# Optimization experiments

Hardware: AMD Instinct MI355X
Metric: run time of the kernel (lower is better)

## Reference

```python
import jax, jax.numpy as jnp
import numpy as np
import math

N_HEAD = 16
N_EMBD = 1024
N_LATENTS = 64
HEAD_DIM = N_EMBD // N_HEAD  # 64
ROPE_THETA = 10000.0


def setup_inputs() -> dict:
    key = jax.random.key(0)
    ks = jax.random.split(key, 6)
    B, T = 4, 4096
    x = jax.random.normal(ks[0], (B, T, N_EMBD), dtype=jnp.float32)
    # torch Linear weights applied as x @ W with W: [in, out] (equivalent up to init)
    s = 1.0 / math.sqrt(N_EMBD)
    Wk = jax.random.normal(ks[1], (N_EMBD, N_EMBD), dtype=jnp.float32) * s
    Wv = jax.random.normal(ks[2], (N_EMBD, N_EMBD), dtype=jnp.float32) * s
    Wg = jax.random.normal(ks[3], (N_EMBD, N_HEAD * N_LATENTS), dtype=jnp.float32) * s
    Wp = jax.random.normal(ks[4], (N_EMBD, N_EMBD), dtype=jnp.float32) * s
    latent_q = jax.random.normal(ks[5], (1, N_LATENTS, N_HEAD, HEAD_DIM), dtype=jnp.float32)
    return {"x": x, "latent_q": latent_q, "Wk": Wk, "Wv": Wv, "Wg": Wg, "Wp": Wp}


def _rope_interleaved(k, theta):
    # k: [B, T, H, D]; interleaved pairs rotated by position-dependent angles
    B, T, H, D = k.shape
    inv_freq = 1.0 / (theta ** (jnp.arange(0, D, 2, dtype=jnp.float32) / D))  # [D/2]
    ang = jnp.arange(T, dtype=jnp.float32)[:, None] * inv_freq[None, :]       # [T, D/2]
    cos = jnp.cos(ang)[None, :, None, :]
    sin = jnp.sin(ang)[None, :, None, :]
    k2 = k.reshape(B, T, H, D // 2, 2)
    kr = jnp.stack([k2[..., 0] * cos - k2[..., 1] * sin,
                    k2[..., 0] * sin + k2[..., 1] * cos], axis=-1)
    return kr.reshape(B, T, H, D).astype(k.dtype)


def reference(x, latent_q, Wk, Wv, Wg, Wp):
    B, T, C = x.shape
    H, D, L = N_HEAD, HEAD_DIM, N_LATENTS
    k = (x @ Wk).reshape(B, T, H, D)
    v = (x @ Wv).reshape(B, T, H, D)
    gates = jax.nn.softmax((x @ Wg).reshape(B, T, H, L), axis=-1)  # [B,T,H,L]
    k = _rope_interleaved(k, ROPE_THETA)
    q = jnp.broadcast_to(latent_q, (B, L, H, D)).transpose(0, 2, 1, 3)  # [B,H,L,D]
    kt = k.transpose(0, 2, 1, 3)  # [B,H,T,D]
    vt = v.transpose(0, 2, 1, 3)  # [B,H,T,D]
    scale = 1.0 / jnp.sqrt(jnp.asarray(D, dtype=x.dtype))
    scores = jnp.einsum('bhld,bhtd->bhlt', q, kt) * scale  # [B,H,L,T]
    # PyTorch SDPA is_causal with L_q != L_kv: top-left aligned tril(ones(L, T))
    causal = jnp.arange(T)[None, :] <= jnp.arange(L)[:, None]  # [L,T]
    scores = jnp.where(causal[None, None], scores, -jnp.inf)
    attn = jax.nn.softmax(scores, axis=-1)
    attn_out = jnp.einsum('bhlt,bhtd->bhld', attn, vt)  # [B,H,L,D]
    gates_t = gates.transpose(0, 2, 1, 3)  # [B,H,T,L]
    weighted = jnp.einsum('bhld,bhtl->bhtd', attn_out, gates_t)  # [B,H,T,D]
    out = weighted.transpose(0, 2, 1, 3).reshape(B, T, C)
    return out @ Wp
```

## Files before the change

### kernel.cpp

```cpp
#include <hip/hip_runtime.h>
#include <hip/hip_bf16.h>


typedef __attribute__((ext_vector_type(8))) short bf16x8;
typedef __attribute__((ext_vector_type(4))) float f32x4;
typedef __attribute__((ext_vector_type(4))) unsigned short us4;
typedef __attribute__((ext_vector_type(8))) unsigned short us8;

__device__ __forceinline__ void gll16(const void* g, void* l) {
  __builtin_amdgcn_global_load_lds((const __attribute__((address_space(1))) void*)g,
                                   (__attribute__((address_space(3))) void*)l, 16, 0, 0);
}

__global__ __launch_bounds__(256)
void prep_kernel(const float* __restrict__ x, __hip_bfloat16* __restrict__ xb,
                 const float* __restrict__ Wg, const float* __restrict__ Wk,
                 const float* __restrict__ Wv, const float* __restrict__ Wp,
                 __hip_bfloat16* __restrict__ WgT, __hip_bfloat16* __restrict__ WkT,
                 __hip_bfloat16* __restrict__ WvT, __hip_bfloat16* __restrict__ WpT) {
  const int bid = blockIdx.x, tid = threadIdx.x;
  if (bid < 2048) {
    const int stride = 2048 * 256;
    for (int i = bid * 256 + tid; i < 4194304; i += stride) {
      float4 f = reinterpret_cast<const float4*>(x)[i];
      union { __hip_bfloat16 h[4]; us4 v; } u;
      u.h[0] = __float2bfloat16(f.x);
      u.h[1] = __float2bfloat16(f.y);
      u.h[2] = __float2bfloat16(f.z);
      u.h[3] = __float2bfloat16(f.w);
      reinterpret_cast<us4*>(xb)[i] = u.v;
    }
  } else {
    const int t = bid - 2048;
    const int z = t >> 10, rem = t & 1023;
    const float* W = (z == 0) ? Wg : ((z == 1) ? Wk : ((z == 2) ? Wv : Wp));
    __hip_bfloat16* Wt = (z == 0) ? WgT : ((z == 1) ? WkT : ((z == 2) ? WvT : WpT));
    __shared__ float tile[32][33];
    const int bx = (rem & 31) * 32, by = (rem >> 5) * 32;
    const int tx = tid & 31, ty = tid >> 5;
    #pragma unroll
    for (int j = 0; j < 32; j += 8)
      tile[ty + j][tx] = W[(size_t)(by + ty + j) * 1024 + bx + tx];
    __syncthreads();
    #pragma unroll
    for (int j = 0; j < 32; j += 8)
      Wt[(size_t)(bx + ty + j) * 1024 + by + tx] = __float2bfloat16(tile[tx][ty + j]);
  }
}

template <int EPI>
__global__ __launch_bounds__(512, 2)
void gemm256(const __hip_bfloat16* __restrict__ A, const __hip_bfloat16* __restrict__ Bt,
             void* __restrict__ Cv, int K, int ldc,
             long long astride, long long bstride, long long cstride) {
  __shared__ __align__(16) unsigned short SA[2][256 * 64];
  __shared__ __align__(16) unsigned short SB[2][256 * 64];
  const int tid = threadIdx.x;
  const int lane = tid & 63;
  const int w = tid >> 6;
  const int wm = w >> 2, wn = w & 3;
  const int lr = lane & 15, lk = lane >> 4;
  const int m0 = blockIdx.x * 256, n0 = blockIdx.y * 256;
  const long long b = blockIdx.z;
  const __hip_bfloat16* Ab = A + b * astride;
  const __hip_bfloat16* Bb = Bt + b * bstride;

  f32x4 acc[8][4] = {};

  const int NT = K >> 6;
  int buf = 0;

  auto STAGE = [&](int bsel, int kt) {
    #pragma unroll
    for (int r = 0; r < 4; ++r) {
      int c = r * 512 + tid;
      int row = c >> 3, slot = c & 7;
      int gch = slot ^ (row & 7);
      gll16(Ab + (size_t)(m0 + row) * K + kt + gch * 8, (char*)&SA[bsel][0] + c * 16);
      gll16(Bb + (size_t)(n0 + row) * K + kt + gch * 8, (char*)&SB[bsel][0] + c * 16);
    }
  };

  STAGE(0, 0);
  __syncthreads();

  for (int t = 0; t < NT; ++t) {
    if (t + 1 < NT) STAGE(buf ^ 1, (t + 1) << 6);

    bf16x8 bfr[2][4];
    #pragma unroll
    for (int kk = 0; kk < 2; ++kk)
      #pragma unroll
      for (int ni = 0; ni < 4; ++ni) {
        int row = wn * 64 + ni * 16 + lr;
        int ch = (kk * 4 + lk) ^ (row & 7);
        bfr[kk][ni] = *(const bf16x8*)&SB[buf][row * 64 + ch * 8];
      }
    #pragma unroll
    for (int mi = 0; mi < 8; ++mi) {
      int row = wm * 128 + mi * 16 + lr;
      int ch0 = lk ^ (row & 7);
      int ch1 = (4 + lk) ^ (row & 7);
      bf16x8 a0 = *(const bf16x8*)&SA[buf][row * 64 + ch0 * 8];
      bf16x8 a1 = *(const bf16x8*)&SA[buf][row * 64 + ch1 * 8];
      #pragma unroll
      for (int ni = 0; ni < 4; ++ni)
        acc[mi][ni] = __builtin_amdgcn_mfma_f32_16x16x32_bf16(a0, bfr[0][ni], acc[mi][ni], 0, 0, 0);
      #pragma unroll
      for (int ni = 0; ni < 4; ++ni)
        acc[mi][ni] = __builtin_amdgcn_mfma_f32_16x16x32_bf16(a1, bfr[1][ni], acc[mi][ni], 0, 0, 0);
    }
    __syncthreads();
    buf ^= 1;
  }

  if (EPI == 0) {
    float* C = (float*)Cv + b * cstride;
    #pragma unroll
    for (int mi = 0; mi < 8; ++mi) {
      int r = m0 + wm * 128 + mi * 16 + lk * 4;
      #pragma unroll
      for (int ni = 0; ni < 4; ++ni) {
        int c = n0 + wn * 64 + ni * 16 + lr;
        #pragma unroll
        for (int jj = 0; jj < 4; ++jj)
          C[(size_t)(r + jj) * ldc + c] = acc[mi][ni][jj];
      }
    }
  } else {
    __hip_bfloat16* C = (__hip_bfloat16*)Cv + b * cstride;
    #pragma unroll
    for (int mi = 0; mi < 8; ++mi) {
      #pragma unroll
      for (int jj = 0; jj < 4; ++jj) {
        float mx = -3.0e38f;
        #pragma unroll
        for (int ni = 0; ni < 4; ++ni) mx = fmaxf(mx, acc[mi][ni][jj]);
        mx = fmaxf(mx, __shfl_xor(mx, 1));
        mx = fmaxf(mx, __shfl_xor(mx, 2));
        mx = fmaxf(mx, __shfl_xor(mx, 4));
        mx = fmaxf(mx, __shfl_xor(mx, 8));
        float e[4];
        float s = 0.f;
        #pragma unroll
        for (int ni = 0; ni < 4; ++ni) { e[ni] = __expf(acc[mi][ni][jj] - mx); s += e[ni]; }
        s += __shfl_xor(s, 1);
        s += __shfl_xor(s, 2);
        s += __shfl_xor(s, 4);
        s += __shfl_xor(s, 8);
        float inv = 1.0f / s;
        int r = m0 + wm * 128 + mi * 16 + lk * 4 + jj;
        #pragma unroll
        for (int ni = 0; ni < 4; ++ni)
          C[(size_t)r * ldc + n0 + wn * 64 + ni * 16 + lr] = __float2bfloat16(e[ni] * inv);
      }
    }
  }
}

__global__ __launch_bounds__(256)
void gemm_kv(const __hip_bfloat16* __restrict__ A, const __hip_bfloat16* __restrict__ Bt,
             float* __restrict__ kvp) {
  __shared__ __align__(16) unsigned short As[128 * 32];
  __shared__ __align__(16) unsigned short Bs[128 * 32];
  const int tid = threadIdx.x;
  const int lane = tid & 63;
  const int w = tid >> 6;
  const int wm = w >> 1, wn = w & 1;
  const int lr = lane & 15, lk = lane >> 4;
  const int m0 = blockIdx.x * 128, n0 = blockIdx.y * 128;
  const int ks = blockIdx.z;
  const int K = 1024;

  f32x4 acc[4][4] = {};
  const int r0 = tid >> 2;
  const int c8 = (tid & 3) * 8;

  auto xrow = [&](int rg) { return (size_t)(rg >> 6) * 4096 + (rg & 63); };

  for (int ki = 0; ki < 4; ++ki) {
    int kt = ks * 128 + ki * 32;
    __syncthreads();
    gll16(A + xrow(m0 + r0) * K + kt + c8,      (char*)As + (w * 64) * 16);
    gll16(Bt + (size_t)(n0 + r0) * K + kt + c8, (char*)Bs + (w * 64) * 16);
    gll16(A + xrow(m0 + 64 + r0) * K + kt + c8,      (char*)As + (256 + w * 64) * 16);
    gll16(Bt + (size_t)(n0 + 64 + r0) * K + kt + c8, (char*)Bs + (256 + w * 64) * 16);
    __syncthreads();

    bf16x8 af[4], bf[4];
    #pragma unroll
    for (int mi = 0; mi < 4; ++mi)
      af[mi] = *(const bf16x8*)&As[(wm * 64 + mi * 16 + lr) * 32 + lk * 8];
    #pragma unroll
    for (int ni = 0; ni < 4; ++ni)
      bf[ni] = *(const bf16x8*)&Bs[(wn * 64 + ni * 16 + lr) * 32 + lk * 8];
    #pragma unroll
    for (int mi = 0; mi < 4; ++mi)
      #pragma unroll
      for (int ni = 0; ni < 4; ++ni)
        acc[mi][ni] = __builtin_amdgcn_mfma_f32_16x16x32_bf16(af[mi], bf[ni], acc[mi][ni], 0, 0, 0);
  }

  float* C = kvp + (size_t)ks * 256 * 2048;
  #pragma unroll
  for (int mi = 0; mi < 4; ++mi) {
    int r = m0 + wm * 64 + mi * 16 + lk * 4;
    #pragma unroll
    for (int ni = 0; ni < 4; ++ni) {
      int c = n0 + wn * 64 + ni * 16 + lr;
      #pragma unroll
      for (int jj = 0; jj < 4; ++jj)
        C[(size_t)(r + jj) * 2048 + c] = acc[mi][ni][jj];
    }
  }
}

__global__ __launch_bounds__(256)
void attn_kernel(const float* __restrict__ kvp, const float* __restrict__ lq,
                 __hip_bfloat16* __restrict__ aoB) {
  const int h = blockIdx.x, b = blockIdx.y;
  __shared__ float Ks[64][64];
  __shared__ float Vs[64][64];
  __shared__ float S[64][65];
  __shared__ float Pt[64][65];
  const int tid = threadIdx.x;

  {
    int r = tid >> 4;
    int c4 = (tid & 15) * 4;
    int i0 = c4 >> 1;
    float inv0 = exp2f(-13.287712379549449f * ((float)i0 * (1.0f / 32.0f)));
    float inv1 = exp2f(-13.287712379549449f * ((float)(i0 + 1) * (1.0f / 32.0f)));
    #pragma unroll
    for (int j = 0; j < 4; ++j) {
      int row = j * 16 + r;
      float4 kf = make_float4(0.f, 0.f, 0.f, 0.f);
      float4 vf = make_float4(0.f, 0.f, 0.f, 0.f);
      #pragma unroll
      for (int ks = 0; ks < 8; ++ks) {
        const float* base = kvp + ((size_t)ks * 256 + b * 64 + row) * 2048 + h * 64;
        float4 kp = *(const float4*)(base + c4);
        float4 vp = *(const float4*)(base + 1024 + c4);
        kf.x += kp.x; kf.y += kp.y; kf.z += kp.z; kf.w += kp.w;
        vf.x += vp.x; vf.y += vp.y; vf.z += vp.z; vf.w += vp.w;
      }
      float a0 = (float)row * inv0, a1 = (float)row * inv1;
      float s0 = sinf(a0), c0 = cosf(a0), s1 = sinf(a1), c1 = cosf(a1);
      *(float4*)&Ks[row][c4] = make_float4(kf.x * c0 - kf.y * s0, kf.x * s0 + kf.y * c0,
                                           kf.z * c1 - kf.w * s1, kf.z * s1 + kf.w * c1);
      *(float4*)&Vs[row][c4] = vf;
    }
  }
  __syncthreads();

  {
    const int w = tid >> 6, l = tid & 63;
    float q[64];
    const float4* lq4 = (const float4*)(lq + ((size_t)l * 16 + h) * 64);
    #pragma unroll
    for (int i = 0; i < 16; ++i) {
      float4 f = lq4[i];
      q[4 * i] = f.x; q[4 * i + 1] = f.y; q[4 * i + 2] = f.z; q[4 * i + 3] = f.w;
    }
    #pragma unroll
    for (int tl = 0; tl < 16; ++tl) {
      int t = w * 16 + tl;
      float a = 0.f;
      #pragma unroll
      for (int d4 = 0; d4 < 16; ++d4) {
        float4 kf = *(const float4*)&Ks[t][d4 * 4];
        a += q[4 * d4] * kf.x + q[4 * d4 + 1] * kf.y + q[4 * d4 + 2] * kf.z + q[4 * d4 + 3] * kf.w;
      }
      S[l][t] = a * 0.125f;
    }
  }
  __syncthreads();

  {
    const int l = tid >> 2, c = tid & 3;
    float sv[16];
    float mx = -3.0e38f;
    #pragma unroll
    for (int i = 0; i < 16; ++i) {
      int t = c * 16 + i;
      sv[i] = S[l][t];
      if (t <= l) mx = fmaxf(mx, sv[i]);
    }
    mx = fmaxf(mx, __shfl_xor(mx, 1));
    mx = fmaxf(mx, __shfl_xor(mx, 2));
    float sum = 0.f;
    float e[16];
    #pragma unroll
    for (int i = 0; i < 16; ++i) {
      int t = c * 16 + i;
      e[i] = (t <= l) ? __expf(sv[i] - mx) : 0.f;
      sum += e[i];
    }
    sum += __shfl_xor(sum, 1);
    sum += __shfl_xor(sum, 2);
    float inv = 1.0f / sum;
    #pragma unroll
    for (int i = 0; i < 16; ++i) Pt[c * 16 + i][l] = e[i] * inv;
  }
  __syncthreads();

  {
    const int w = tid >> 6, l = tid & 63;
    float o[16];
    #pragma unroll
    for (int i = 0; i < 16; ++i) o[i] = 0.f;
    for (int t = 0; t < 64; ++t) {
      float p = Pt[t][l];
      #pragma unroll
      for (int d4 = 0; d4 < 4; ++d4) {
        float4 vf = *(const float4*)&Vs[t][w * 16 + d4 * 4];
        o[4 * d4]     += p * vf.x;
        o[4 * d4 + 1] += p * vf.y;
        o[4 * d4 + 2] += p * vf.z;
        o[4 * d4 + 3] += p * vf.w;
      }
    }
    union { __hip_bfloat16 h[16]; us8 v[2]; } u;
    #pragma unroll
    for (int i = 0; i < 16; ++i) u.h[i] = __float2bfloat16(o[i]);
    us8* dst = (us8*)(aoB + (((size_t)b * 16 + h) * 64 + l) * 64 + w * 16);
    dst[0] = u.v[0];
    dst[1] = u.v[1];
  }
}

__global__ __launch_bounds__(256)
void build_mt_mfma(const __hip_bfloat16* __restrict__ aoB, const __hip_bfloat16* __restrict__ WpT,
                   __hip_bfloat16* __restrict__ Mt) {
  __shared__ __align__(16) unsigned short SW[256 * 64];
  __shared__ __align__(16) unsigned short SAo[64 * 64];
  const int ct = blockIdx.x, h = blockIdx.y, b = blockIdx.z;
  const int tid = threadIdx.x;
  const int lane = tid & 63;
  const int w = tid >> 6;
  const int lr = lane & 15, lk = lane >> 4;

  #pragma unroll
  for (int j = 0; j < 8; ++j) {
    int c2 = j * 256 + tid;
    int row = c2 >> 3, slot = c2 & 7;
    int gch = slot ^ (row & 7);
    gll16(WpT + (size_t)(ct * 256 + row) * 1024 + h * 64 + gch * 8, (char*)SW + c2 * 16);
  }
  const __hip_bfloat16* aob = aoB + (((size_t)b * 16 + h) * 64) * 64;
  #pragma unroll
  for (int j = 0; j < 2; ++j) {
    int c2 = j * 256 + tid;
    int row = c2 >> 3, slot = c2 & 7;
    int gch = slot ^ (row & 7);
    gll16(aob + (size_t)row * 64 + gch * 8, (char*)SAo + c2 * 16);
  }
  __syncthreads();

  f32x4 acc[4][4] = {};
  bf16x8 bfr[2][4];
  #pragma unroll
  for (int kk = 0; kk < 2; ++kk)
    #pragma unroll
    for (int ni = 0; ni < 4; ++ni) {
      int row = ni * 16 + lr;
      int ch = (kk * 4 + lk) ^ (row & 7);
      bfr[kk][ni] = *(const bf16x8*)&SAo[row * 64 + ch * 8];
    }
  #pragma unroll
  for (int mi = 0; mi < 4; ++mi) {
    int row = w * 64 + mi * 16 + lr;
    int ch0 = lk ^ (row & 7);
    int ch1 = (4 + lk) ^ (row & 7);
    bf16x8 a0 = *(const bf16x8*)&SW[row * 64 + ch0 * 8];
    bf16x8 a1 = *(const bf16x8*)&SW[row * 64 + ch1 * 8];
    #pragma unroll
    for (int ni = 0; ni < 4; ++ni)
      acc[mi][ni] = __builtin_amdgcn_mfma_f32_16x16x32_bf16(a0, bfr[0][ni], acc[mi][ni], 0, 0, 0);
    #pragma unroll
    for (int ni = 0; ni < 4; ++ni)
      acc[mi][ni] = __builtin_amdgcn_mfma_f32_16x16x32_bf16(a1, bfr[1][ni], acc[mi][ni], 0, 0, 0);
  }

  #pragma unroll
  for (int mi = 0; mi < 4; ++mi) {
    int c = ct * 256 + w * 64 + mi * 16 + lk * 4;
    #pragma unroll
    for (int ni = 0; ni < 4; ++ni) {
      int l = ni * 16 + lr;
      #pragma unroll
      for (int jj = 0; jj < 4; ++jj)
        Mt[((size_t)b * 1024 + c + jj) * 1024 + h * 64 + l] = __float2bfloat16(acc[mi][ni][jj]);
    }
  }
}

extern "C" void kernel_launch(void* const* d_in, const int* in_sizes, int n_in,
                              void* d_out, int out_size, void* d_ws, size_t ws_size,
                              hipStream_t stream) {
  const float* x  = (const float*)d_in[0];
  const float* lq = (const float*)d_in[1];
  const float* Wk = (const float*)d_in[2];
  const float* Wv = (const float*)d_in[3];
  const float* Wg = (const float*)d_in[4];
  const float* Wp = (const float*)d_in[5];
  float* out = (float*)d_out;

  char* w = (char*)d_ws;
  __hip_bfloat16* xb   = (__hip_bfloat16*)(w);
  __hip_bfloat16* G    = (__hip_bfloat16*)(w + 33554432);
  __hip_bfloat16* WgT  = (__hip_bfloat16*)(w + 67108864);
  __hip_bfloat16* WkvT = (__hip_bfloat16*)(w + 69206016);
  __hip_bfloat16* WpT  = (__hip_bfloat16*)(w + 73400320);
  __hip_bfloat16* Mt   = (__hip_bfloat16*)(w + 75497472);
  __hip_bfloat16* aoB  = (__hip_bfloat16*)(w + 83886080);
  float* kvp = out;

  prep_kernel<<<6144, 256, 0, stream>>>(x, xb, Wg, Wk, Wv, Wp,
                                        WgT, WkvT, WkvT + 1024 * 1024, WpT);

  gemm256<1><<<dim3(64, 4, 1), 512, 0, stream>>>(xb, WgT, G, 1024, 1024, 0LL, 0LL, 0LL);

  gemm_kv<<<dim3(2, 16, 8), 256, 0, stream>>>(xb, WkvT, kvp);

  attn_kernel<<<dim3(16, 4), 256, 0, stream>>>(kvp, lq, aoB);

  build_mt_mfma<<<dim3(4, 16, 4), 256, 0, stream>>>(aoB, WpT, Mt);

  gemm256<0><<<dim3(16, 4, 4), 512, 0, stream>>>(G, Mt, out, 1024, 1024,
                                                 4096LL * 1024, 1024LL * 1024, 4096LL * 1024);
}
```

Measured before the change: 132.3 us.

## Fuse fp32-to-bf16 conversion of x into gates and KV GEMM loaders

Removes the separate pass that converted x to a bf16 workspace copy. The gates GEMM now stages fp32 x tiles into LDS via direct global-to-LDS loads and converts them to bf16 in shared memory inside a double-buffered pipeline. The KV GEMM loads fp32 x into registers and converts before writing LDS. This drops the 32MB bf16 write and reread of x, but doubles the bytes each GEMM reads for A, adds LDS usage, and the gates kernel loses its 2-blocks occupancy hint and uses a smaller K tile.

```diff
diff --git a/kernel.cpp b/kernel.cpp
--- a/kernel.cpp
+++ b/kernel.cpp
@@ -13,46 +13,150 @@
 }
 
 __global__ __launch_bounds__(256)
-void prep_kernel(const float* __restrict__ x, __hip_bfloat16* __restrict__ xb,
-                 const float* __restrict__ Wg, const float* __restrict__ Wk,
-                 const float* __restrict__ Wv, const float* __restrict__ Wp,
-                 __hip_bfloat16* __restrict__ WgT, __hip_bfloat16* __restrict__ WkT,
-                 __hip_bfloat16* __restrict__ WvT, __hip_bfloat16* __restrict__ WpT) {
+void prep4(const float* __restrict__ Wg, const float* __restrict__ Wk,
+           const float* __restrict__ Wv, const float* __restrict__ Wp,
+           __hip_bfloat16* __restrict__ WgT, __hip_bfloat16* __restrict__ WkT,
+           __hip_bfloat16* __restrict__ WvT, __hip_bfloat16* __restrict__ WpT) {
   const int bid = blockIdx.x, tid = threadIdx.x;
-  if (bid < 2048) {
-    const int stride = 2048 * 256;
-    for (int i = bid * 256 + tid; i < 4194304; i += stride) {
-      float4 f = reinterpret_cast<const float4*>(x)[i];
-      union { __hip_bfloat16 h[4]; us4 v; } u;
-      u.h[0] = __float2bfloat16(f.x);
-      u.h[1] = __float2bfloat16(f.y);
-      u.h[2] = __float2bfloat16(f.z);
-      u.h[3] = __float2bfloat16(f.w);
-      reinterpret_cast<us4*>(xb)[i] = u.v;
-    }
-  } else {
-    const int t = bid - 2048;
-    const int z = t >> 10, rem = t & 1023;
-    const float* W = (z == 0) ? Wg : ((z == 1) ? Wk : ((z == 2) ? Wv : Wp));
-    __hip_bfloat16* Wt = (z == 0) ? WgT : ((z == 1) ? WkT : ((z == 2) ? WvT : WpT));
-    __shared__ float tile[32][33];
-    const int bx = (rem & 31) * 32, by = (rem >> 5) * 32;
-    const int tx = tid & 31, ty = tid >> 5;
-    #pragma unroll
-    for (int j = 0; j < 32; j += 8)
-      tile[ty + j][tx] = W[(size_t)(by + ty + j) * 1024 + bx + tx];
+  const int z = bid >> 10, rem = bid & 1023;
+  const float* W = (z == 0) ? Wg : ((z == 1) ? Wk : ((z == 2) ? Wv : Wp));
+  __hip_bfloat16* Wt = (z == 0) ? WgT : ((z == 1) ? WkT : ((z == 2) ? WvT : WpT));
+  __shared__ float tile[32][33];
+  const int bx = (rem & 31) * 32, by = (rem >> 5) * 32;
+  const int tx = tid & 31, ty = tid >> 5;
+  #pragma unroll
+  for (int j = 0; j < 32; j += 8)
+    tile[ty + j][tx] = W[(size_t)(by + ty + j) * 1024 + bx + tx];
+  __syncthreads();
+  #pragma unroll
+  for (int j = 0; j < 32; j += 8)
+    Wt[(size_t)(bx + ty + j) * 1024 + by + tx] = __float2bfloat16(tile[tx][ty + j]);
+}
+
+__global__ __launch_bounds__(512)
+void gemm_gates_f32(const float* __restrict__ X, const __hip_bfloat16* __restrict__ Bt,
+                    __hip_bfloat16* __restrict__ G) {
+  __shared__ __align__(16) float SF[2][256 * 32];
+  __shared__ __align__(16) unsigned short SA16[2][256 * 32];
+  __shared__ __align__(16) unsigned short SB[2][256 * 32];
+  const int tid = threadIdx.x;
+  const int lane = tid & 63;
+  const int w = tid >> 6;
+  const int wm = w >> 2, wn = w & 3;
+  const int lr = lane & 15, lk = lane >> 4;
+  const int m0 = blockIdx.x * 256, n0 = blockIdx.y * 256;
+  const int K = 1024;
+
+  f32x4 acc[8][4] = {};
+
+  auto stageF = [&](int bsel, int kt) {
+    #pragma unroll
+    for (int r = 0; r < 4; ++r) {
+      int c = r * 512 + tid;
+      int row = c >> 3, p = c & 7;
+      int gs = p ^ (row & 7);
+      gll16(X + (size_t)(m0 + row) * K + kt + gs * 4, (char*)&SF[bsel][0] + c * 16);
+    }
+  };
+  auto stageB = [&](int bsel, int kt) {
+    #pragma unroll
+    for (int r = 0; r < 2; ++r) {
+      int c = r * 512 + tid;
+      int row2 = c >> 3, p = c & 7;
+      int l = p ^ (row2 & 7);
+      int row = row2 * 2 + (l >> 2);
+      int s4 = l & 3;
+      gll16(Bt + (size_t)(n0 + row) * K + kt + s4 * 8, (char*)&SB[bsel][0] + c * 16);
+    }
+  };
+  auto convert = [&](int bsel) {
+    #pragma unroll
+    for (int r = 0; r < 2; ++r) {
+      int c = r * 512 + tid;
+      int row2 = c >> 3, p = c & 7;
+      int l = p ^ (row2 & 7);
+      int row = row2 * 2 + (l >> 2);
+      int s4 = l & 3;
+      int f0 = (2 * s4) ^ (row & 7);
+      int f1 = (2 * s4 + 1) ^ (row & 7);
+      float4 a  = *(const float4*)&SF[bsel][row * 32 + f0 * 4];
+      float4 b2 = *(const float4*)&SF[bsel][row * 32 + f1 * 4];
+      union { __hip_bfloat16 h[8]; bf16x8 v; } pk;
+      pk.h[0] = __float2bfloat16(a.x);  pk.h[1] = __float2bfloat16(a.y);
+      pk.h[2] = __float2bfloat16(a.z);  pk.h[3] = __float2bfloat16(a.w);
+      pk.h[4] = __float2bfloat16(b2.x); pk.h[5] = __float2bfloat16(b2.y);
+      pk.h[6] = __float2bfloat16(b2.z); pk.h[7] = __float2bfloat16(b2.w);
+      *(bf16x8*)&SA16[bsel][c * 8] = pk.v;
+    }
+  };
+
+  stageF(0, 0);
+  stageB(0, 0);
+  __syncthreads();
+  convert(0);
+  stageF(1, 32);
+  __syncthreads();
+
+  const int NT = 32;
+  for (int t = 0; t < NT; ++t) {
+    if (t + 2 < NT) stageF(t & 1, (t + 2) * 32);
+    if (t + 1 < NT) {
+      stageB((t + 1) & 1, (t + 1) * 32);
+      convert((t + 1) & 1);
+    }
+
+    const int buf = t & 1;
+    bf16x8 bfr[4];
+    #pragma unroll
+    for (int ni = 0; ni < 4; ++ni) {
+      int row = wn * 64 + ni * 16 + lr;
+      int ch = ((row >> 1) * 8) + ((((row & 1) << 2) | lk) ^ ((row >> 1) & 7));
+      bfr[ni] = *(const bf16x8*)&SB[buf][ch * 8];
+    }
+    #pragma unroll
+    for (int mi = 0; mi < 8; ++mi) {
+      int row = wm * 128 + mi * 16 + lr;
+      int ch = ((row >> 1) * 8) + ((((row & 1) << 2) | lk) ^ ((row >> 1) & 7));
+      bf16x8 a = *(const bf16x8*)&SA16[buf][ch * 8];
+      #pragma unroll
+      for (int ni = 0; ni < 4; ++ni)
+        acc[mi][ni] = __builtin_amdgcn_mfma_f32_16x16x32_bf16(a, bfr[ni], acc[mi][ni], 0, 0, 0);
+    }
     __syncthreads();
-    #pragma unroll
-    for (int j = 0; j < 32; j += 8)
-      Wt[(size_t)(bx + ty + j) * 1024 + by + tx] = __float2bfloat16(tile[tx][ty + j]);
-  }
-}
-
-template <int EPI>
+  }
+
+  #pragma unroll
+  for (int mi = 0; mi < 8; ++mi) {
+    #pragma unroll
+    for (int jj = 0; jj < 4; ++jj) {
+      float mx = -3.0e38f;
+      #pragma unroll
+      for (int ni = 0; ni < 4; ++ni) mx = fmaxf(mx, acc[mi][ni][jj]);
+      mx = fmaxf(mx, __shfl_xor(mx, 1));
+      mx = fmaxf(mx, __shfl_xor(mx, 2));
+      mx = fmaxf(mx, __shfl_xor(mx, 4));
+      mx = fmaxf(mx, __shfl_xor(mx, 8));
+      float e[4];
+      float s = 0.f;
+      #pragma unroll
+      for (int ni = 0; ni < 4; ++ni) { e[ni] = __expf(acc[mi][ni][jj] - mx); s += e[ni]; }
+      s += __shfl_xor(s, 1);
+      s += __shfl_xor(s, 2);
+      s += __shfl_xor(s, 4);
+      s += __shfl_xor(s, 8);
+      float inv = 1.0f / s;
+      int r = m0 + wm * 128 + mi * 16 + lk * 4 + jj;
+      #pragma unroll
+      for (int ni = 0; ni < 4; ++ni)
+        G[(size_t)r * 1024 + n0 + wn * 64 + ni * 16 + lr] = __float2bfloat16(e[ni] * inv);
+    }
+  }
+}
+
 __global__ __launch_bounds__(512, 2)
-void gemm256(const __hip_bfloat16* __restrict__ A, const __hip_bfloat16* __restrict__ Bt,
-             void* __restrict__ Cv, int K, int ldc,
-             long long astride, long long bstride, long long cstride) {
+void gemm256o(const __hip_bfloat16* __restrict__ A, const __hip_bfloat16* __restrict__ Bt,
+              float* __restrict__ Cv, int K, int ldc,
+              long long astride, long long bstride, long long cstride) {
   __shared__ __align__(16) unsigned short SA[2][256 * 64];
   __shared__ __align__(16) unsigned short SB[2][256 * 64];
   const int tid = threadIdx.x;
@@ -114,52 +218,22 @@
     buf ^= 1;
   }
 
-  if (EPI == 0) {
-    float* C = (float*)Cv + b * cstride;
-    #pragma unroll
-    for (int mi = 0; mi < 8; ++mi) {
-      int r = m0 + wm * 128 + mi * 16 + lk * 4;
-      #pragma unroll
-      for (int ni = 0; ni < 4; ++ni) {
-        int c = n0 + wn * 64 + ni * 16 + lr;
-        #pragma unroll
-        for (int jj = 0; jj < 4; ++jj)
-          C[(size_t)(r + jj) * ldc + c] = acc[mi][ni][jj];
-      }
-    }
-  } else {
-    __hip_bfloat16* C = (__hip_bfloat16*)Cv + b * cstride;
-    #pragma unroll
-    for (int mi = 0; mi < 8; ++mi) {
-      #pragma unroll
-      for (int jj = 0; jj < 4; ++jj) {
-        float mx = -3.0e38f;
-        #pragma unroll
-        for (int ni = 0; ni < 4; ++ni) mx = fmaxf(mx, acc[mi][ni][jj]);
-        mx = fmaxf(mx, __shfl_xor(mx, 1));
-        mx = fmaxf(mx, __shfl_xor(mx, 2));
-        mx = fmaxf(mx, __shfl_xor(mx, 4));
-        mx = fmaxf(mx, __shfl_xor(mx, 8));
-        float e[4];
-        float s = 0.f;
-        #pragma unroll
-        for (int ni = 0; ni < 4; ++ni) { e[ni] = __expf(acc[mi][ni][jj] - mx); s += e[ni]; }
-        s += __shfl_xor(s, 1);
-        s += __shfl_xor(s, 2);
-        s += __shfl_xor(s, 4);
-        s += __shfl_xor(s, 8);
-        float inv = 1.0f / s;
-        int r = m0 + wm * 128 + mi * 16 + lk * 4 + jj;
-        #pragma unroll
-        for (int ni = 0; ni < 4; ++ni)
-          C[(size_t)r * ldc + n0 + wn * 64 + ni * 16 + lr] = __float2bfloat16(e[ni] * inv);
-      }
+  float* C = Cv + b * cstride;
+  #pragma unroll
+  for (int mi = 0; mi < 8; ++mi) {
+    int r = m0 + wm * 128 + mi * 16 + lk * 4;
+    #pragma unroll
+    for (int ni = 0; ni < 4; ++ni) {
+      int c = n0 + wn * 64 + ni * 16 + lr;
+      #pragma unroll
+      for (int jj = 0; jj < 4; ++jj)
+        C[(size_t)(r + jj) * ldc + c] = acc[mi][ni][jj];
     }
   }
 }
 
 __global__ __launch_bounds__(256)
-void gemm_kv(const __hip_bfloat16* __restrict__ A, const __hip_bfloat16* __restrict__ Bt,
+void gemm_kv(const float* __restrict__ X, const __hip_bfloat16* __restrict__ Bt,
              float* __restrict__ kvp) {
   __shared__ __align__(16) unsigned short As[128 * 32];
   __shared__ __align__(16) unsigned short Bs[128 * 32];
@@ -173,18 +247,36 @@
   const int K = 1024;
 
   f32x4 acc[4][4] = {};
-  const int r0 = tid >> 2;
-  const int c8 = (tid & 3) * 8;
 
   auto xrow = [&](int rg) { return (size_t)(rg >> 6) * 4096 + (rg & 63); };
 
   for (int ki = 0; ki < 4; ++ki) {
     int kt = ks * 128 + ki * 32;
     __syncthreads();
-    gll16(A + xrow(m0 + r0) * K + kt + c8,      (char*)As + (w * 64) * 16);
-    gll16(Bt + (size_t)(n0 + r0) * K + kt + c8, (char*)Bs + (w * 64) * 16);
-    gll16(A + xrow(m0 + 64 + r0) * K + kt + c8,      (char*)As + (256 + w * 64) * 16);
-    gll16(Bt + (size_t)(n0 + 64 + r0) * K + kt + c8, (char*)Bs + (256 + w * 64) * 16);
+    float4 av[4];
+    #pragma unroll
+    for (int r = 0; r < 2; ++r) {
+      int c = r * 256 + tid;
+      int row = c >> 2, s = c & 3;
+      const float* src = X + xrow(m0 + row) * K + kt + s * 8;
+      av[2 * r]     = *(const float4*)src;
+      av[2 * r + 1] = *(const float4*)(src + 4);
+    }
+    #pragma unroll
+    for (int r = 0; r < 2; ++r) {
+      int c = r * 256 + tid;
+      int row = c >> 2, s = c & 3;
+      gll16(Bt + (size_t)(n0 + row) * K + kt + s * 8, (char*)Bs + c * 16);
+    }
+    #pragma unroll
+    for (int r = 0; r < 2; ++r) {
+      int c = r * 256 + tid;
+      union { __hip_bfloat16 h[8]; bf16x8 v; } p;
+      const float* f = (const float*)&av[2 * r];
+      #pragma unroll
+      for (int e = 0; e < 8; ++e) p.h[e] = __float2bfloat16(f[e]);
+      *(bf16x8*)((char*)As + c * 16) = p.v;
+    }
     __syncthreads();
 
     bf16x8 af[4], bf[4];
@@ -407,26 +499,24 @@
   float* out = (float*)d_out;
 
   char* w = (char*)d_ws;
-  __hip_bfloat16* xb   = (__hip_bfloat16*)(w);
-  __hip_bfloat16* G    = (__hip_bfloat16*)(w + 33554432);
-  __hip_bfloat16* WgT  = (__hip_bfloat16*)(w + 67108864);
-  __hip_bfloat16* WkvT = (__hip_bfloat16*)(w + 69206016);
-  __hip_bfloat16* WpT  = (__hip_bfloat16*)(w + 73400320);
-  __hip_bfloat16* Mt   = (__hip_bfloat16*)(w + 75497472);
-  __hip_bfloat16* aoB  = (__hip_bfloat16*)(w + 83886080);
+  __hip_bfloat16* G    = (__hip_bfloat16*)(w);
+  __hip_bfloat16* WgT  = (__hip_bfloat16*)(w + 33554432);
+  __hip_bfloat16* WkvT = (__hip_bfloat16*)(w + 35651584);
+  __hip_bfloat16* WpT  = (__hip_bfloat16*)(w + 39845888);
+  __hip_bfloat16* Mt   = (__hip_bfloat16*)(w + 41943040);
+  __hip_bfloat16* aoB  = (__hip_bfloat16*)(w + 50331648);
   float* kvp = out;
 
-  prep_kernel<<<6144, 256, 0, stream>>>(x, xb, Wg, Wk, Wv, Wp,
-                                        WgT, WkvT, WkvT + 1024 * 1024, WpT);
-
-  gemm256<1><<<dim3(64, 4, 1), 512, 0, stream>>>(xb, WgT, G, 1024, 1024, 0LL, 0LL, 0LL);
-
-  gemm_kv<<<dim3(2, 16, 8), 256, 0, stream>>>(xb, WkvT, kvp);
+  prep4<<<4096, 256, 0, stream>>>(Wg, Wk, Wv, Wp, WgT, WkvT, WkvT + 1024 * 1024, WpT);
+
+  gemm_gates_f32<<<dim3(64, 4), 512, 0, stream>>>(x, WgT, G);
+
+  gemm_kv<<<dim3(2, 16, 8), 256, 0, stream>>>(x, WkvT, kvp);
 
   attn_kernel<<<dim3(16, 4), 256, 0, stream>>>(kvp, lq, aoB);
 
   build_mt_mfma<<<dim3(4, 16, 4), 256, 0, stream>>>(aoB, WpT, Mt);
 
-  gemm256<0><<<dim3(16, 4, 4), 512, 0, stream>>>(G, Mt, out, 1024, 1024,
-                                                 4096LL * 1024, 1024LL * 1024, 4096LL * 1024);
-}
+  gemm256o<<<dim3(16, 4, 4), 512, 0, stream>>>(G, Mt, out, 1024, 1024,
+                                               4096LL * 1024, 1024LL * 1024, 4096LL * 1024);
+}
```

Measured after the change: 137.1 us. +3.6%, slower.

## Fuse attention into Mt construction and swizzle GEMM block order

Applied to the files above, without the earlier changes.

Merges the attention kernel with the build-Mt kernel, so each block recomputes attention output for its (b,h) and writes it into shared memory instead of a global bf16 buffer. This removes one launch and the global round trip of the attention output. The attention work is now done redundantly four times, once per column tile. Separately, the two gemm256 launches switch to a 1D grid with an XCD-aware block swizzle (bid&7)*32+(bid>>3), aimed at better L2 locality across chiplets.

```diff
diff --git a/kernel.cpp b/kernel.cpp
--- a/kernel.cpp
+++ b/kernel.cpp
@@ -5,7 +5,6 @@
 typedef __attribute__((ext_vector_type(8))) short bf16x8;
 typedef __attribute__((ext_vector_type(4))) float f32x4;
 typedef __attribute__((ext_vector_type(4))) unsigned short us4;
-typedef __attribute__((ext_vector_type(8))) unsigned short us8;
 
 __device__ __forceinline__ void gll16(const void* g, void* l) {
   __builtin_amdgcn_global_load_lds((const __attribute__((address_space(1))) void*)g,
@@ -52,7 +51,8 @@
 __global__ __launch_bounds__(512, 2)
 void gemm256(const __hip_bfloat16* __restrict__ A, const __hip_bfloat16* __restrict__ Bt,
              void* __restrict__ Cv, int K, int ldc,
-             long long astride, long long bstride, long long cstride) {
+             long long astride, long long bstride, long long cstride,
+             int nx, int ny) {
   __shared__ __align__(16) unsigned short SA[2][256 * 64];
   __shared__ __align__(16) unsigned short SB[2][256 * 64];
   const int tid = threadIdx.x;
@@ -60,8 +60,14 @@
   const int w = tid >> 6;
   const int wm = w >> 2, wn = w & 3;
   const int lr = lane & 15, lk = lane >> 4;
-  const int m0 = blockIdx.x * 256, n0 = blockIdx.y * 256;
-  const long long b = blockIdx.z;
+
+  const int bid = blockIdx.x;
+  const int swz = (bid & 7) * 32 + (bid >> 3);
+  const int ix = swz % nx;
+  const int iy = (swz / nx) % ny;
+  const long long b = swz / (nx * ny);
+  const int m0 = ix * 256, n0 = iy * 256;
+
   const __hip_bfloat16* Ab = A + b * astride;
   const __hip_bfloat16* Bb = Bt + b * bstride;
 
@@ -216,14 +222,27 @@
 }
 
 __global__ __launch_bounds__(256)
-void attn_kernel(const float* __restrict__ kvp, const float* __restrict__ lq,
-                 __hip_bfloat16* __restrict__ aoB) {
-  const int h = blockIdx.x, b = blockIdx.y;
+void attn_mt(const float* __restrict__ kvp, const float* __restrict__ lq,
+             const __hip_bfloat16* __restrict__ WpT, __hip_bfloat16* __restrict__ Mt) {
+  const int ct = blockIdx.x, h = blockIdx.y, b = blockIdx.z;
   __shared__ float Ks[64][64];
   __shared__ float Vs[64][64];
   __shared__ float S[64][65];
   __shared__ float Pt[64][65];
+  __shared__ __align__(16) unsigned short SW[256 * 64];
+  __shared__ __align__(16) unsigned short SAo[64 * 64];
   const int tid = threadIdx.x;
+  const int lane = tid & 63;
+  const int w = tid >> 6;
+  const int lr = lane & 15, lk = lane >> 4;
+
+  #pragma unroll
+  for (int j = 0; j < 8; ++j) {
+    int c2 = j * 256 + tid;
+    int row = c2 >> 3, slot = c2 & 7;
+    int gch = slot ^ (row & 7);
+    gll16(WpT + (size_t)(ct * 256 + row) * 1024 + h * 64 + gch * 8, (char*)SW + c2 * 16);
+  }
 
   {
     int r = tid >> 4;
@@ -254,7 +273,7 @@
   __syncthreads();
 
   {
-    const int w = tid >> 6, l = tid & 63;
+    const int l = tid & 63;
     float q[64];
     const float4* lq4 = (const float4*)(lq + ((size_t)l * 16 + h) * 64);
     #pragma unroll
@@ -305,7 +324,7 @@
   __syncthreads();
 
   {
-    const int w = tid >> 6, l = tid & 63;
+    const int l = tid & 63;
     float o[16];
     #pragma unroll
     for (int i = 0; i < 16; ++i) o[i] = 0.f;
@@ -320,40 +339,11 @@
         o[4 * d4 + 3] += p * vf.w;
       }
     }
-    union { __hip_bfloat16 h[16]; us8 v[2]; } u;
-    #pragma unroll
-    for (int i = 0; i < 16; ++i) u.h[i] = __float2bfloat16(o[i]);
-    us8* dst = (us8*)(aoB + (((size_t)b * 16 + h) * 64 + l) * 64 + w * 16);
-    dst[0] = u.v[0];
-    dst[1] = u.v[1];
-  }
-}
-
-__global__ __launch_bounds__(256)
-void build_mt_mfma(const __hip_bfloat16* __restrict__ aoB, const __hip_bfloat16* __restrict__ WpT,
-                   __hip_bfloat16* __restrict__ Mt) {
-  __shared__ __align__(16) unsigned short SW[256 * 64];
-  __shared__ __align__(16) unsigned short SAo[64 * 64];
-  const int ct = blockIdx.x, h = blockIdx.y, b = blockIdx.z;
-  const int tid = threadIdx.x;
-  const int lane = tid & 63;
-  const int w = tid >> 6;
-  const int lr = lane & 15, lk = lane >> 4;
-
-  #pragma unroll
-  for (int j = 0; j < 8; ++j) {
-    int c2 = j * 256 + tid;
-    int row = c2 >> 3, slot = c2 & 7;
-    int gch = slot ^ (row & 7);
-    gll16(WpT + (size_t)(ct * 256 + row) * 1024 + h * 64 + gch * 8, (char*)SW + c2 * 16);
-  }
-  const __hip_bfloat16* aob = aoB + (((size_t)b * 16 + h) * 64) * 64;
-  #pragma unroll
-  for (int j = 0; j < 2; ++j) {
-    int c2 = j * 256 + tid;
-    int row = c2 >> 3, slot = c2 & 7;
-    int gch = slot ^ (row & 7);
-    gll16(aob + (size_t)row * 64 + gch * 8, (char*)SAo + c2 * 16);
+    union { __hip_bfloat16 hh[8]; bf16x8 v; } p0, p1;
+    #pragma unroll
+    for (int i = 0; i < 8; ++i) { p0.hh[i] = __float2bfloat16(o[i]); p1.hh[i] = __float2bfloat16(o[8 + i]); }
+    *(bf16x8*)&SAo[l * 64 + ((2 * w) ^ (l & 7)) * 8]     = p0.v;
+    *(bf16x8*)&SAo[l * 64 + ((2 * w + 1) ^ (l & 7)) * 8] = p1.v;
   }
   __syncthreads();
 
@@ -413,20 +403,17 @@
   __hip_bfloat16* WkvT = (__hip_bfloat16*)(w + 69206016);
   __hip_bfloat16* WpT  = (__hip_bfloat16*)(w + 73400320);
   __hip_bfloat16* Mt   = (__hip_bfloat16*)(w + 75497472);
-  __hip_bfloat16* aoB  = (__hip_bfloat16*)(w + 83886080);
   float* kvp = out;
 
   prep_kernel<<<6144, 256, 0, stream>>>(x, xb, Wg, Wk, Wv, Wp,
                                         WgT, WkvT, WkvT + 1024 * 1024, WpT);
 
-  gemm256<1><<<dim3(64, 4, 1), 512, 0, stream>>>(xb, WgT, G, 1024, 1024, 0LL, 0LL, 0LL);
+  gemm256<1><<<256, 512, 0, stream>>>(xb, WgT, G, 1024, 1024, 0LL, 0LL, 0LL, 64, 4);
 
   gemm_kv<<<dim3(2, 16, 8), 256, 0, stream>>>(xb, WkvT, kvp);
 
-  attn_kernel<<<dim3(16, 4), 256, 0, stream>>>(kvp, lq, aoB);
-
-  build_mt_mfma<<<dim3(4, 16, 4), 256, 0, stream>>>(aoB, WpT, Mt);
-
-  gemm256<0><<<dim3(16, 4, 4), 512, 0, stream>>>(G, Mt, out, 1024, 1024,
-                                                 4096LL * 1024, 1024LL * 1024, 4096LL * 1024);
-}
+  attn_mt<<<dim3(4, 16, 4), 256, 0, stream>>>(kvp, lq, WpT, Mt);
+
+  gemm256<0><<<256, 512, 0, stream>>>(G, Mt, out, 1024, 1024,
+                                      4096LL * 1024, 1024LL * 1024, 4096LL * 1024, 16, 4);
+}
```

Result: slower. 136.8 us (+3.4%).
